# Kernel tuning notes

Measured on AMD Instinct MI355X. Metric: run time of the kernel, lower is better.

## Reference

```python
import jax, jax.numpy as jnp
import numpy as np

D_MODEL = 768
N_HEADS = 12
D_K = D_MODEL // N_HEADS

def setup_inputs() -> dict:
    key = jax.random.key(0)
    ks = jax.random.split(key, 9)
    B, S = 4, 2048
    s = 1.0 / np.sqrt(D_MODEL)
    return {
        "x": jax.random.normal(ks[0], (B, S, D_MODEL), dtype=jnp.float32),
        "Wq": jax.random.normal(ks[1], (D_MODEL, D_MODEL), dtype=jnp.float32) * s,
        "bq": jnp.zeros((D_MODEL,), dtype=jnp.float32),
        "Wk": jax.random.normal(ks[2], (D_MODEL, D_MODEL), dtype=jnp.float32) * s,
        "bk": jnp.zeros((D_MODEL,), dtype=jnp.float32),
        "Wv": jax.random.normal(ks[3], (D_MODEL, D_MODEL), dtype=jnp.float32) * s,
        "bv": jnp.zeros((D_MODEL,), dtype=jnp.float32),
        "Wo": jax.random.normal(ks[4], (D_MODEL, D_MODEL), dtype=jnp.float32) * s,
        "bo": jnp.zeros((D_MODEL,), dtype=jnp.float32),
    }

def reference(x, Wq, bq, Wk, bk, Wv, bv, Wo, bo):
    B, S, _ = x.shape
    # projections (nn.Linear: x @ W^T + b; here weights stored as (in, out) so x @ W + b)
    q = x @ Wq + bq
    k = x @ Wk + bk
    v = x @ Wv + bv
    # split heads -> (B, H, S, d_k)
    q = q.reshape(B, S, N_HEADS, D_K).transpose(0, 2, 1, 3)
    k = k.reshape(B, S, N_HEADS, D_K).transpose(0, 2, 1, 3)
    v = v.reshape(B, S, N_HEADS, D_K).transpose(0, 2, 1, 3)
    scores = jnp.einsum('bhqd,bhkd->bhqk', q, k) / jnp.sqrt(jnp.float32(D_K))
    causal = jnp.tril(jnp.ones((S, S), dtype=bool))  # True = keep
    scores = jnp.where(causal, scores, jnp.finfo(scores.dtype).min)
    weights = jax.nn.softmax(scores, axis=-1)  # dropout is identity in eval
    out = jnp.einsum('bhqk,bhkd->bhqd', weights, v)
    out = out.transpose(0, 2, 1, 3).reshape(B, S, D_MODEL)
    return out @ Wo + bo
```

## Files before the change

### kernel.cpp

```cpp
#include <hip/hip_runtime.h>
#include <hip/hip_bf16.h>

#define DM    768
#define HEADS 12
#define DK    64
#define SEQ   2048
#define BATCH 4
#define NE    ((size_t)BATCH * SEQ * DM)
#define KT    12
#define BRICK 8192

typedef short v8s __attribute__((ext_vector_type(8)));
typedef float v4f __attribute__((ext_vector_type(4)));

#define LDS_PTR(p) ((__attribute__((address_space(3))) unsigned int*)(p))
#define GLB_PTR(p) ((const __attribute__((address_space(1))) unsigned int*)(p))

__device__ __forceinline__ unsigned short f2bf(float f) {
    union { float f; unsigned u; } v; v.f = f;
    unsigned r = (v.u + 0x7FFFu + ((v.u >> 16) & 1u)) >> 16;
    return (unsigned short)r;
}
__device__ __forceinline__ unsigned pk2(float a, float b) {
    union { float f; unsigned u; } x, y; x.f = a; y.f = b;
    return (x.u >> 16) | (y.u & 0xFFFF0000u);
}
__device__ __forceinline__ unsigned pk2r(float a, float b) {
    return (unsigned)f2bf(a) | ((unsigned)f2bf(b) << 16);
}
__device__ __forceinline__ float fexp2(float x) {
#if __has_builtin(__builtin_amdgcn_exp2f)
    return __builtin_amdgcn_exp2f(x);
#else
    return __expf(x * 0.69314718056f);
#endif
}

#define QSCALE 0.18033688011112042f

__global__ __launch_bounds__(256)
void cvt_x_kernel(const float* __restrict__ x, unsigned short* __restrict__ xb) {
    const size_t p = ((size_t)blockIdx.x * 256 + threadIdx.x) * 8;
    const int m = (int)(p / DM);
    const int k = (int)(p % DM);
    const float4 a = *(const float4*)(x + p);
    const float4 b = *(const float4*)(x + p + 4);
    v8s o;
    o[0] = (short)f2bf(a.x); o[1] = (short)f2bf(a.y);
    o[2] = (short)f2bf(a.z); o[3] = (short)f2bf(a.w);
    o[4] = (short)f2bf(b.x); o[5] = (short)f2bf(b.y);
    o[6] = (short)f2bf(b.z); o[7] = (short)f2bf(b.w);
    const size_t dst = ((size_t)(m >> 7) * KT + (k >> 6)) * BRICK + (size_t)(m & 127) * 64 + (k & 63);
    *(v8s*)(xb + dst) = o;
}

__global__ __launch_bounds__(256)
void cvt_w_kernel(const float* __restrict__ W0, const float* __restrict__ W1,
                  const float* __restrict__ W2, const float* __restrict__ W3,
                  unsigned short* __restrict__ wt) {
    __shared__ unsigned short T[64][72];
    const int z = blockIdx.z;
    const float* W = (z == 0) ? W0 : (z == 1) ? W1 : (z == 2) ? W2 : W3;
    const float scale = (z == 0) ? QSCALE : 1.0f;
    const int k0 = blockIdx.x * 64, n0 = blockIdx.y * 64;
    const int t = threadIdx.x;
    {
        const int kr = t >> 2;
        const int ns = (t & 3) * 16;
        #pragma unroll
        for (int j = 0; j < 4; ++j) {
            const float4 v = *(const float4*)(W + (size_t)(k0 + kr) * DM + n0 + ns + j * 4);
            T[ns + j * 4 + 0][kr] = f2bf(v.x * scale);
            T[ns + j * 4 + 1][kr] = f2bf(v.y * scale);
            T[ns + j * 4 + 2][kr] = f2bf(v.z * scale);
            T[ns + j * 4 + 3][kr] = f2bf(v.w * scale);
        }
    }
    __syncthreads();
    {
        unsigned short* dst = wt + (size_t)z * DM * DM +
            ((size_t)(n0 >> 7) * KT + (k0 >> 6)) * BRICK + (size_t)(n0 & 64) * 64;
        const int n = t >> 2;
        const int ks = (t & 3) * 16;
        #pragma unroll
        for (int j = 0; j < 2; ++j)
            *(v8s*)(dst + (size_t)n * 64 + ks + j * 8) = *(const v8s*)&T[n][ks + j * 8];
    }
}

__global__ __launch_bounds__(256)
void gemm_qkv_kernel(const unsigned short* __restrict__ xb, const unsigned short* __restrict__ wtbuf,
                     const float* __restrict__ bq, const float* __restrict__ bk,
                     const float* __restrict__ bv,
                     unsigned short* __restrict__ qb, unsigned short* __restrict__ kb,
                     unsigned short* __restrict__ vtb) {
    __shared__ unsigned short smem[32768];
    const int idx = blockIdx.x;
    const int xcd = idx & 7, g = idx >> 3;
    const int mb = xcd + 8 * (g & 7);
    const int yb = g >> 3;
    const int z = yb / 6;
    const int N0 = (yb % 6) * 128;
    const float* bias = (z == 0) ? bq : (z == 1) ? bk : bv;
    const float bscale = (z == 0) ? QSCALE : 1.0f;

    const int t = threadIdx.x;
    const int w = t >> 6, lane = t & 63, quad = lane >> 4, l15 = lane & 15;
    const int wm = w >> 1, wn = w & 1;
    const int M0 = mb * 128;

    const unsigned short* gA = xb + (size_t)mb * (KT * BRICK);
    const unsigned short* gB = wtbuf + (size_t)yb * (KT * BRICK);

    const int r8 = lane >> 3;
    const int c8 = (lane & 7) ^ r8;
    const int goff = r8 * 64 + c8 * 8;
    const int rl = l15 & 7, rh = l15 >> 3;

    v4f acc[4][4];
    #pragma unroll
    for (int i = 0; i < 4; ++i)
        #pragma unroll
        for (int j = 0; j < 4; ++j) acc[i][j] = (v4f){0, 0, 0, 0};

    #pragma unroll
    for (int u = 0; u < 4; ++u) {
        const int win = w * 4 + u;
        __builtin_amdgcn_global_load_lds(GLB_PTR(gA + win * 512 + goff), LDS_PTR(smem + win * 512), 16, 0, 0);
        __builtin_amdgcn_global_load_lds(GLB_PTR(gB + win * 512 + goff), LDS_PTR(smem + 16384 + win * 512), 16, 0, 0);
    }
    __syncthreads();

    for (int kt = 0; kt < KT; ++kt) {
        const int cur = kt & 1;
        if (kt + 1 < KT) {
            const unsigned short* ta = gA + (kt + 1) * BRICK;
            const unsigned short* tb = gB + (kt + 1) * BRICK;
            const int nb = (1 - cur) * 8192;
            #pragma unroll
            for (int u = 0; u < 4; ++u) {
                const int win = w * 4 + u;
                __builtin_amdgcn_global_load_lds(GLB_PTR(ta + win * 512 + goff), LDS_PTR(smem + nb + win * 512), 16, 0, 0);
                __builtin_amdgcn_global_load_lds(GLB_PTR(tb + win * 512 + goff), LDS_PTR(smem + 16384 + nb + win * 512), 16, 0, 0);
            }
        }
        const unsigned short* As = smem + cur * 8192;
        const unsigned short* Bs = smem + 16384 + cur * 8192;
        #pragma unroll
        for (int kc = 0; kc < 2; ++kc) {
            const int cs = ((kc << 2) | quad) ^ rl;
            v8s a[4], b[4];
            #pragma unroll
            for (int i = 0; i < 4; ++i)
                a[i] = *(const v8s*)&As[(wm * 8 + i * 2 + rh) * 512 + rl * 64 + cs * 8];
            #pragma unroll
            for (int j = 0; j < 4; ++j)
                b[j] = *(const v8s*)&Bs[(wn * 8 + j * 2 + rh) * 512 + rl * 64 + cs * 8];
            #pragma unroll
            for (int i = 0; i < 4; ++i)
                #pragma unroll
                for (int j = 0; j < 4; ++j)
                    acc[i][j] = __builtin_amdgcn_mfma_f32_16x16x32_bf16(a[i], b[j], acc[i][j], 0, 0, 0);
        }
        __syncthreads();
    }

    const int b_ = M0 >> 11;
    const int sidx0 = M0 & 2047;
    const int h0 = N0 >> 6;

    if (z < 2) {
        unsigned short* outp = (z == 0) ? qb : kb;
        #pragma unroll
        for (int j = 0; j < 4; ++j) {
            const int n = N0 + wn * 64 + j * 16 + l15;
            const int h = n >> 6, d = n & 63;
            const float bv_ = bias[n] * bscale;
            #pragma unroll
            for (int i = 0; i < 4; ++i)
                #pragma unroll
                for (int r = 0; r < 4; ++r) {
                    const int sidx = sidx0 + wm * 64 + i * 16 + quad * 4 + r;
                    outp[(((size_t)(b_ * HEADS + h) * SEQ + sidx) << 6) + d] = f2bf(acc[i][j][r] + bv_);
                }
        }
    } else {
        unsigned short* Ts = smem;
        #pragma unroll
        for (int p = 0; p < 2; ++p) {
            __syncthreads();
            if (wm == p) {
                #pragma unroll
                for (int j = 0; j < 4; ++j) {
                    const int dloc = wn * 64 + j * 16 + l15;
                    const float bv_ = bias[N0 + dloc];
                    #pragma unroll
                    for (int i = 0; i < 4; ++i)
                        #pragma unroll
                        for (int r = 0; r < 4; ++r)
                            Ts[dloc * 72 + i * 16 + quad * 4 + r] = f2bf(acc[i][j][r] + bv_);
                }
            }
            __syncthreads();
            const int dloc = t >> 1, ms = (t & 1) * 32;
            const int h = h0 + (dloc >> 6), d = dloc & 63;
            unsigned short* dst = vtb + (((size_t)(b_ * HEADS + h) * DK + d) << 11) + sidx0 + p * 64 + ms;
            #pragma unroll
            for (int jj = 0; jj < 4; ++jj)
                *(v8s*)(dst + jj * 8) = *(const v8s*)&Ts[dloc * 72 + ms + jj * 8];
        }
    }
}

__global__ __launch_bounds__(256)
void gemm_out_kernel(const unsigned short* __restrict__ ob, const unsigned short* __restrict__ wto,
                     const float* __restrict__ bias, float* __restrict__ out) {
    __shared__ unsigned short smem[32768];
    const int idx = blockIdx.x;
    const int xcd = idx & 7, g = idx >> 3;
    const int mb = xcd + 8 * (g & 7);
    const int nb = g >> 3;
    const int t = threadIdx.x;
    const int w = t >> 6, lane = t & 63, quad = lane >> 4, l15 = lane & 15;
    const int wm = w >> 1, wn = w & 1;
    const int M0 = mb * 128;
    const int N0 = nb * 128;

    const unsigned short* gA = ob + (size_t)mb * (KT * BRICK);
    const unsigned short* gB = wto + (size_t)nb * (KT * BRICK);

    const int r8 = lane >> 3;
    const int c8 = (lane & 7) ^ r8;
    const int goff = r8 * 64 + c8 * 8;
    const int rl = l15 & 7, rh = l15 >> 3;

    v4f acc[4][4];
    #pragma unroll
    for (int i = 0; i < 4; ++i)
        #pragma unroll
        for (int j = 0; j < 4; ++j) acc[i][j] = (v4f){0, 0, 0, 0};

    #pragma unroll
    for (int u = 0; u < 4; ++u) {
        const int win = w * 4 + u;
        __builtin_amdgcn_global_load_lds(GLB_PTR(gA + win * 512 + goff), LDS_PTR(smem + win * 512), 16, 0, 0);
        __builtin_amdgcn_global_load_lds(GLB_PTR(gB + win * 512 + goff), LDS_PTR(smem + 16384 + win * 512), 16, 0, 0);
    }
    __syncthreads();

    for (int kt = 0; kt < KT; ++kt) {
        const int cur = kt & 1;
        if (kt + 1 < KT) {
            const unsigned short* ta = gA + (kt + 1) * BRICK;
            const unsigned short* tb = gB + (kt + 1) * BRICK;
            const int nxt = (1 - cur) * 8192;
            #pragma unroll
            for (int u = 0; u < 4; ++u) {
                const int win = w * 4 + u;
                __builtin_amdgcn_global_load_lds(GLB_PTR(ta + win * 512 + goff), LDS_PTR(smem + nxt + win * 512), 16, 0, 0);
                __builtin_amdgcn_global_load_lds(GLB_PTR(tb + win * 512 + goff), LDS_PTR(smem + 16384 + nxt + win * 512), 16, 0, 0);
            }
        }
        const unsigned short* As = smem + cur * 8192;
        const unsigned short* Bs = smem + 16384 + cur * 8192;
        #pragma unroll
        for (int kc = 0; kc < 2; ++kc) {
            const int cs = ((kc << 2) | quad) ^ rl;
            v8s a[4], b[4];
            #pragma unroll
            for (int i = 0; i < 4; ++i)
                a[i] = *(const v8s*)&As[(wm * 8 + i * 2 + rh) * 512 + rl * 64 + cs * 8];
            #pragma unroll
            for (int j = 0; j < 4; ++j)
                b[j] = *(const v8s*)&Bs[(wn * 8 + j * 2 + rh) * 512 + rl * 64 + cs * 8];
            #pragma unroll
            for (int i = 0; i < 4; ++i)
                #pragma unroll
                for (int j = 0; j < 4; ++j)
                    acc[i][j] = __builtin_amdgcn_mfma_f32_16x16x32_bf16(a[i], b[j], acc[i][j], 0, 0, 0);
        }
        __syncthreads();
    }

    #pragma unroll
    for (int j = 0; j < 4; ++j) {
        const int n = N0 + wn * 64 + j * 16 + l15;
        const float bv_ = bias[n];
        #pragma unroll
        for (int i = 0; i < 4; ++i)
            #pragma unroll
            for (int r = 0; r < 4; ++r) {
                const int m = M0 + wm * 64 + i * 16 + quad * 4 + r;
                out[(size_t)m * DM + n] = acc[i][j][r] + bv_;
            }
    }
}

__global__ __launch_bounds__(256, 3)
void attn_kernel(const unsigned short* __restrict__ Q, const unsigned short* __restrict__ K,
                 const unsigned short* __restrict__ VT, unsigned short* __restrict__ O) {
    __shared__ unsigned short Kb[2][64][72];
    __shared__ unsigned short Vb[2][64][72];
    __shared__ unsigned short Ps[4][16][72];
    const int t = threadIdx.x;
    const int w = t >> 6, lane = t & 63, quad = lane >> 4, l15 = lane & 15;

    const int idx = blockIdx.x;
    const int xcd = idx & 7;
    const int j   = idx >> 3;
    const int bh  = xcd + 8 * (j >> 4);
    const int s   = j & 15;
    const int sA  = s, sB = 31 - s;
    const int q0A = sA * 64, q0B = sB * 64;
    const int nkt = sB + 1;
    const size_t kvbase = (size_t)bh * SEQ * DK;

    v8s qfA[2], qfB[2];
    #pragma unroll
    for (int c = 0; c < 2; ++c) {
        qfA[c] = *(const v8s*)(Q + kvbase + (size_t)(q0A + w * 16 + l15) * DK + c * 32 + quad * 8);
        qfB[c] = *(const v8s*)(Q + kvbase + (size_t)(q0B + w * 16 + l15) * DK + c * 32 + quad * 8);
    }

    v4f oA[4], oB[4];
    #pragma unroll
    for (int nf = 0; nf < 4; ++nf) { oA[nf] = (v4f){0,0,0,0}; oB[nf] = (v4f){0,0,0,0}; }
    float lsA = 0.f, lsB = 0.f;

    const int srow = t >> 3;
    const int scol = (t & 7) * 8;

    v8s kr0 = *(const v8s*)(K  + kvbase + (size_t)srow * DK + scol);
    v8s kr1 = *(const v8s*)(K  + kvbase + (size_t)(srow + 32) * DK + scol);
    v8s vr0 = *(const v8s*)(VT + kvbase + ((size_t)srow << 11) + scol);
    v8s vr1 = *(const v8s*)(VT + kvbase + ((size_t)(srow + 32) << 11) + scol);
    *(v8s*)&Kb[0][srow][scol]      = kr0;
    *(v8s*)&Kb[0][srow + 32][scol] = kr1;
    *(v8s*)&Vb[0][srow][scol]      = vr0;
    *(v8s*)&Vb[0][srow + 32][scol] = vr1;
    __syncthreads();

    const int qA = q0A + w * 16 + l15;
    const int qB = q0B + w * 16 + l15;

    for (int kt = 0; kt < nkt; ++kt) {
        const int k0 = kt * 64;
        const int cur = kt & 1;
        if (kt + 1 < nkt) {
            const int kn = k0 + 64;
            kr0 = *(const v8s*)(K  + kvbase + (size_t)(kn + srow) * DK + scol);
            kr1 = *(const v8s*)(K  + kvbase + (size_t)(kn + srow + 32) * DK + scol);
            vr0 = *(const v8s*)(VT + kvbase + ((size_t)srow << 11) + kn + scol);
            vr1 = *(const v8s*)(VT + kvbase + ((size_t)(srow + 32) << 11) + kn + scol);
        }

        const bool actA = (kt <= sA);

        v4f scB[4], scA[4];
        #pragma unroll
        for (int s4 = 0; s4 < 4; ++s4) { scB[s4] = (v4f){0,0,0,0}; scA[s4] = (v4f){0,0,0,0}; }
        #pragma unroll
        for (int c = 0; c < 2; ++c)
            #pragma unroll
            for (int s4 = 0; s4 < 4; ++s4) {
                const v8s kf = *(const v8s*)&Kb[cur][s4 * 16 + l15][c * 32 + quad * 8];
                scB[s4] = __builtin_amdgcn_mfma_f32_16x16x32_bf16(kf, qfB[c], scB[s4], 0, 0, 0);
                if (actA)
                    scA[s4] = __builtin_amdgcn_mfma_f32_16x16x32_bf16(kf, qfA[c], scA[s4], 0, 0, 0);
            }

        {
            const bool msk = (kt == nkt - 1);
            #pragma unroll
            for (int s4 = 0; s4 < 4; ++s4) {
                float p[4];
                #pragma unroll
                for (int r = 0; r < 4; ++r) {
                    const int key = k0 + s4 * 16 + quad * 4 + r;
                    const float e = fexp2(scB[s4][r]);
                    p[r] = (!msk || key <= qB) ? e : 0.f;
                    lsB += p[r];
                }
                uint2 pkv; pkv.x = pk2(p[0], p[1]); pkv.y = pk2(p[2], p[3]);
                *(uint2*)&Ps[w][l15][s4 * 16 + quad * 4] = pkv;
            }
            #pragma unroll
            for (int kc = 0; kc < 2; ++kc) {
                const v8s pf = *(const v8s*)&Ps[w][l15][kc * 32 + quad * 8];
                #pragma unroll
                for (int nf = 0; nf < 4; ++nf) {
                    const v8s vf = *(const v8s*)&Vb[cur][nf * 16 + l15][kc * 32 + quad * 8];
                    oB[nf] = __builtin_amdgcn_mfma_f32_16x16x32_bf16(vf, pf, oB[nf], 0, 0, 0);
                }
            }
        }

        if (actA) {
            const bool msk = (kt == sA);
            #pragma unroll
            for (int s4 = 0; s4 < 4; ++s4) {
                float p[4];
                #pragma unroll
                for (int r = 0; r < 4; ++r) {
                    const int key = k0 + s4 * 16 + quad * 4 + r;
                    const float e = fexp2(scA[s4][r]);
                    p[r] = (!msk || key <= qA) ? e : 0.f;
                    lsA += p[r];
                }
                uint2 pkv; pkv.x = pk2(p[0], p[1]); pkv.y = pk2(p[2], p[3]);
                *(uint2*)&Ps[w][l15][s4 * 16 + quad * 4] = pkv;
            }
            #pragma unroll
            for (int kc = 0; kc < 2; ++kc) {
                const v8s pf = *(const v8s*)&Ps[w][l15][kc * 32 + quad * 8];
                #pragma unroll
                for (int nf = 0; nf < 4; ++nf) {
                    const v8s vf = *(const v8s*)&Vb[cur][nf * 16 + l15][kc * 32 + quad * 8];
                    oA[nf] = __builtin_amdgcn_mfma_f32_16x16x32_bf16(vf, pf, oA[nf], 0, 0, 0);
                }
            }
        }

        if (kt + 1 < nkt) {
            const int nxt = 1 - cur;
            *(v8s*)&Kb[nxt][srow][scol]      = kr0;
            *(v8s*)&Kb[nxt][srow + 32][scol] = kr1;
            *(v8s*)&Vb[nxt][srow][scol]      = vr0;
            *(v8s*)&Vb[nxt][srow + 32][scol] = vr1;
        }
        __syncthreads();
    }

    lsA += __shfl_xor(lsA, 16); lsA += __shfl_xor(lsA, 32);
    lsB += __shfl_xor(lsB, 16); lsB += __shfl_xor(lsB, 32);
    const float invA = 1.f / lsA, invB = 1.f / lsB;

    const int b = bh / HEADS, h = bh % HEADS;
    const size_t brA = ((size_t)(b * 16 + (q0A >> 7)) * KT + h) * BRICK;
    const size_t brB = ((size_t)(b * 16 + (q0B >> 7)) * KT + h) * BRICK;
    const int rowlA = (q0A & 127) + w * 16 + l15;
    const int rowlB = (q0B & 127) + w * 16 + l15;
    #pragma unroll
    for (int nf = 0; nf < 4; ++nf) {
        uint2 a2, b2;
        a2.x = pk2r(oA[nf][0] * invA, oA[nf][1] * invA);
        a2.y = pk2r(oA[nf][2] * invA, oA[nf][3] * invA);
        b2.x = pk2r(oB[nf][0] * invB, oB[nf][1] * invB);
        b2.y = pk2r(oB[nf][2] * invB, oB[nf][3] * invB);
        *(uint2*)(O + brA + (size_t)rowlA * 64 + nf * 16 + quad * 4) = a2;
        *(uint2*)(O + brB + (size_t)rowlB * 64 + nf * 16 + quad * 4) = b2;
    }
}

extern "C" void kernel_launch(void* const* d_in, const int* in_sizes, int n_in,
                              void* d_out, int out_size, void* d_ws, size_t ws_size,
                              hipStream_t stream) {
    const float* x  = (const float*)d_in[0];
    const float* Wq = (const float*)d_in[1];
    const float* bq = (const float*)d_in[2];
    const float* Wk = (const float*)d_in[3];
    const float* bk = (const float*)d_in[4];
    const float* Wv = (const float*)d_in[5];
    const float* bv = (const float*)d_in[6];
    const float* Wo = (const float*)d_in[7];
    const float* bo = (const float*)d_in[8];
    float* out = (float*)d_out;

    unsigned short* xb  = (unsigned short*)d_ws;
    unsigned short* qb  = xb  + NE;
    unsigned short* kb  = qb  + NE;
    unsigned short* vtb = kb  + NE;
    unsigned short* wt  = vtb + NE;
    unsigned short* ob  = xb;

    cvt_x_kernel<<<dim3(NE / (8 * 256)), 256, 0, stream>>>(x, xb);
    cvt_w_kernel<<<dim3(12, 12, 4), 256, 0, stream>>>(Wq, Wk, Wv, Wo, wt);
    gemm_qkv_kernel<<<dim3(1152), 256, 0, stream>>>(xb, wt, bq, bk, bv, qb, kb, vtb);
    attn_kernel<<<dim3(768), 256, 0, stream>>>(qb, kb, vtb, ob);
    gemm_out_kernel<<<dim3(384), 256, 0, stream>>>(ob, wt + (size_t)3 * DM * DM, bo, out);
}
```

Baseline: 219.3 us.

## Compute softmax row sums via MFMA with ones vector and hoist V fragment loads

```diff
diff --git a/kernel.cpp b/kernel.cpp
--- a/kernel.cpp
+++ b/kernel.cpp
@@ -325,7 +325,10 @@
     v4f oA[4], oB[4];
     #pragma unroll
     for (int nf = 0; nf < 4; ++nf) { oA[nf] = (v4f){0,0,0,0}; oB[nf] = (v4f){0,0,0,0}; }
-    float lsA = 0.f, lsB = 0.f;
+    v4f osA = (v4f){0,0,0,0}, osB = (v4f){0,0,0,0};
+
+    const short one_bf = (short)0x3F80;
+    const v8s ones = (v8s){one_bf, one_bf, one_bf, one_bf, one_bf, one_bf, one_bf, one_bf};
 
     const int srow = t >> 3;
     const int scol = (t & 7) * 8;
@@ -369,17 +372,26 @@
                     scA[s4] = __builtin_amdgcn_mfma_f32_16x16x32_bf16(kf, qfA[c], scA[s4], 0, 0, 0);
             }
 
+        v8s vfc[2][4];
+        #pragma unroll
+        for (int kc = 0; kc < 2; ++kc)
+            #pragma unroll
+            for (int nf = 0; nf < 4; ++nf)
+                vfc[kc][nf] = *(const v8s*)&Vb[cur][nf * 16 + l15][kc * 32 + quad * 8];
+
         {
             const bool msk = (kt == nkt - 1);
             #pragma unroll
             for (int s4 = 0; s4 < 4; ++s4) {
                 float p[4];
                 #pragma unroll
-                for (int r = 0; r < 4; ++r) {
-                    const int key = k0 + s4 * 16 + quad * 4 + r;
-                    const float e = fexp2(scB[s4][r]);
-                    p[r] = (!msk || key <= qB) ? e : 0.f;
-                    lsB += p[r];
+                for (int r = 0; r < 4; ++r) p[r] = fexp2(scB[s4][r]);
+                if (msk) {
+                    #pragma unroll
+                    for (int r = 0; r < 4; ++r) {
+                        const int key = k0 + s4 * 16 + quad * 4 + r;
+                        if (key > qB) p[r] = 0.f;
+                    }
                 }
                 uint2 pkv; pkv.x = pk2(p[0], p[1]); pkv.y = pk2(p[2], p[3]);
                 *(uint2*)&Ps[w][l15][s4 * 16 + quad * 4] = pkv;
@@ -387,11 +399,10 @@
             #pragma unroll
             for (int kc = 0; kc < 2; ++kc) {
                 const v8s pf = *(const v8s*)&Ps[w][l15][kc * 32 + quad * 8];
-                #pragma unroll
-                for (int nf = 0; nf < 4; ++nf) {
-                    const v8s vf = *(const v8s*)&Vb[cur][nf * 16 + l15][kc * 32 + quad * 8];
-                    oB[nf] = __builtin_amdgcn_mfma_f32_16x16x32_bf16(vf, pf, oB[nf], 0, 0, 0);
-                }
+                osB = __builtin_amdgcn_mfma_f32_16x16x32_bf16(ones, pf, osB, 0, 0, 0);
+                #pragma unroll
+                for (int nf = 0; nf < 4; ++nf)
+                    oB[nf] = __builtin_amdgcn_mfma_f32_16x16x32_bf16(vfc[kc][nf], pf, oB[nf], 0, 0, 0);
             }
         }
 
@@ -401,11 +412,13 @@
             for (int s4 = 0; s4 < 4; ++s4) {
                 float p[4];
                 #pragma unroll
-                for (int r = 0; r < 4; ++r) {
-                    const int key = k0 + s4 * 16 + quad * 4 + r;
-                    const float e = fexp2(scA[s4][r]);
-                    p[r] = (!msk || key <= qA) ? e : 0.f;
-                    lsA += p[r];
+                for (int r = 0; r < 4; ++r) p[r] = fexp2(scA[s4][r]);
+                if (msk) {
+                    #pragma unroll
+                    for (int r = 0; r < 4; ++r) {
+                        const int key = k0 + s4 * 16 + quad * 4 + r;
+                        if (key > qA) p[r] = 0.f;
+                    }
                 }
                 uint2 pkv; pkv.x = pk2(p[0], p[1]); pkv.y = pk2(p[2], p[3]);
                 *(uint2*)&Ps[w][l15][s4 * 16 + quad * 4] = pkv;
@@ -413,11 +426,10 @@
             #pragma unroll
             for (int kc = 0; kc < 2; ++kc) {
                 const v8s pf = *(const v8s*)&Ps[w][l15][kc * 32 + quad * 8];
-                #pragma unroll
-                for (int nf = 0; nf < 4; ++nf) {
-                    const v8s vf = *(const v8s*)&Vb[cur][nf * 16 + l15][kc * 32 + quad * 8];
-                    oA[nf] = __builtin_amdgcn_mfma_f32_16x16x32_bf16(vf, pf, oA[nf], 0, 0, 0);
-                }
+                osA = __builtin_amdgcn_mfma_f32_16x16x32_bf16(ones, pf, osA, 0, 0, 0);
+                #pragma unroll
+                for (int nf = 0; nf < 4; ++nf)
+                    oA[nf] = __builtin_amdgcn_mfma_f32_16x16x32_bf16(vfc[kc][nf], pf, oA[nf], 0, 0, 0);
             }
         }
 
@@ -431,9 +443,7 @@
         __syncthreads();
     }
 
-    lsA += __shfl_xor(lsA, 16); lsA += __shfl_xor(lsA, 32);
-    lsB += __shfl_xor(lsB, 16); lsB += __shfl_xor(lsB, 32);
-    const float invA = 1.f / lsA, invB = 1.f / lsB;
+    const float invA = 1.f / osA[0], invB = 1.f / osB[0];
 
     const int b = bh / HEADS, h = bh % HEADS;
     const size_t brA = ((size_t)(b * 16 + (q0A >> 7)) * KT + h) * BRICK;
```

Result: faster. 206.5 us (-5.8%).

## Split attention into one query tile per block with swizzled LDS and MFMA row sums

Applied to the files above, without the earlier changes.

```diff
diff --git a/kernel.cpp b/kernel.cpp
--- a/kernel.cpp
+++ b/kernel.cpp
@@ -296,159 +296,132 @@
     }
 }
 
-__global__ __launch_bounds__(256, 3)
+__global__ __launch_bounds__(256, 4)
 void attn_kernel(const unsigned short* __restrict__ Q, const unsigned short* __restrict__ K,
                  const unsigned short* __restrict__ VT, unsigned short* __restrict__ O) {
-    __shared__ unsigned short Kb[2][64][72];
-    __shared__ unsigned short Vb[2][64][72];
-    __shared__ unsigned short Ps[4][16][72];
+    __shared__ unsigned short Kb[2][64][64];
+    __shared__ unsigned short Vb[2][64][64];
+    __shared__ unsigned short Ps[4][16][64];
     const int t = threadIdx.x;
     const int w = t >> 6, lane = t & 63, quad = lane >> 4, l15 = lane & 15;
+    const int e7 = l15 & 7;
 
     const int idx = blockIdx.x;
     const int xcd = idx & 7;
-    const int j   = idx >> 3;
-    const int bh  = xcd + 8 * (j >> 4);
-    const int s   = j & 15;
-    const int sA  = s, sB = 31 - s;
-    const int q0A = sA * 64, q0B = sB * 64;
-    const int nkt = sB + 1;
+    const int g   = idx >> 3;
+    const int bh  = xcd + 8 * (g % 6);
+    const int s   = 31 - g / 6;
+    const int q0  = s * 64;
+    const int nkt = s + 1;
     const size_t kvbase = (size_t)bh * SEQ * DK;
 
-    v8s qfA[2], qfB[2];
-    #pragma unroll
-    for (int c = 0; c < 2; ++c) {
-        qfA[c] = *(const v8s*)(Q + kvbase + (size_t)(q0A + w * 16 + l15) * DK + c * 32 + quad * 8);
-        qfB[c] = *(const v8s*)(Q + kvbase + (size_t)(q0B + w * 16 + l15) * DK + c * 32 + quad * 8);
-    }
-
-    v4f oA[4], oB[4];
-    #pragma unroll
-    for (int nf = 0; nf < 4; ++nf) { oA[nf] = (v4f){0,0,0,0}; oB[nf] = (v4f){0,0,0,0}; }
-    float lsA = 0.f, lsB = 0.f;
+    v8s qf[2];
+    #pragma unroll
+    for (int c = 0; c < 2; ++c)
+        qf[c] = *(const v8s*)(Q + kvbase + (size_t)(q0 + w * 16 + l15) * DK + c * 32 + quad * 8);
+
+    v4f o[4];
+    #pragma unroll
+    for (int nf = 0; nf < 4; ++nf) o[nf] = (v4f){0, 0, 0, 0};
+    v4f os = (v4f){0, 0, 0, 0};
+    const v4f zero4 = (v4f){0, 0, 0, 0};
+
+    const short one_bf = (short)0x3F80;
+    const v8s ones = (v8s){one_bf, one_bf, one_bf, one_bf, one_bf, one_bf, one_bf, one_bf};
 
     const int srow = t >> 3;
-    const int scol = (t & 7) * 8;
-
-    v8s kr0 = *(const v8s*)(K  + kvbase + (size_t)srow * DK + scol);
-    v8s kr1 = *(const v8s*)(K  + kvbase + (size_t)(srow + 32) * DK + scol);
-    v8s vr0 = *(const v8s*)(VT + kvbase + ((size_t)srow << 11) + scol);
-    v8s vr1 = *(const v8s*)(VT + kvbase + ((size_t)(srow + 32) << 11) + scol);
-    *(v8s*)&Kb[0][srow][scol]      = kr0;
-    *(v8s*)&Kb[0][srow + 32][scol] = kr1;
-    *(v8s*)&Vb[0][srow][scol]      = vr0;
-    *(v8s*)&Vb[0][srow + 32][scol] = vr1;
+    const int sc16 = t & 7;
+    const int scolsw = (sc16 ^ (srow & 7)) * 8;
+    const int gcol = sc16 * 8;
+
+    v8s kr0 = *(const v8s*)(K  + kvbase + (size_t)srow * DK + gcol);
+    v8s kr1 = *(const v8s*)(K  + kvbase + (size_t)(srow + 32) * DK + gcol);
+    v8s vr0 = *(const v8s*)(VT + kvbase + ((size_t)srow << 11) + gcol);
+    v8s vr1 = *(const v8s*)(VT + kvbase + ((size_t)(srow + 32) << 11) + gcol);
+    *(v8s*)&Kb[0][srow][scolsw]      = kr0;
+    *(v8s*)&Kb[0][srow + 32][scolsw] = kr1;
+    *(v8s*)&Vb[0][srow][scolsw]      = vr0;
+    *(v8s*)&Vb[0][srow + 32][scolsw] = vr1;
     __syncthreads();
 
-    const int qA = q0A + w * 16 + l15;
-    const int qB = q0B + w * 16 + l15;
+    const int q_ = q0 + w * 16 + l15;
 
     for (int kt = 0; kt < nkt; ++kt) {
         const int k0 = kt * 64;
         const int cur = kt & 1;
         if (kt + 1 < nkt) {
             const int kn = k0 + 64;
-            kr0 = *(const v8s*)(K  + kvbase + (size_t)(kn + srow) * DK + scol);
-            kr1 = *(const v8s*)(K  + kvbase + (size_t)(kn + srow + 32) * DK + scol);
-            vr0 = *(const v8s*)(VT + kvbase + ((size_t)srow << 11) + kn + scol);
-            vr1 = *(const v8s*)(VT + kvbase + ((size_t)(srow + 32) << 11) + kn + scol);
-        }
-
-        const bool actA = (kt <= sA);
-
-        v4f scB[4], scA[4];
-        #pragma unroll
-        for (int s4 = 0; s4 < 4; ++s4) { scB[s4] = (v4f){0,0,0,0}; scA[s4] = (v4f){0,0,0,0}; }
-        #pragma unroll
-        for (int c = 0; c < 2; ++c)
-            #pragma unroll
-            for (int s4 = 0; s4 < 4; ++s4) {
-                const v8s kf = *(const v8s*)&Kb[cur][s4 * 16 + l15][c * 32 + quad * 8];
-                scB[s4] = __builtin_amdgcn_mfma_f32_16x16x32_bf16(kf, qfB[c], scB[s4], 0, 0, 0);
-                if (actA)
-                    scA[s4] = __builtin_amdgcn_mfma_f32_16x16x32_bf16(kf, qfA[c], scA[s4], 0, 0, 0);
-            }
+            kr0 = *(const v8s*)(K  + kvbase + (size_t)(kn + srow) * DK + gcol);
+            kr1 = *(const v8s*)(K  + kvbase + (size_t)(kn + srow + 32) * DK + gcol);
+            vr0 = *(const v8s*)(VT + kvbase + ((size_t)srow << 11) + kn + gcol);
+            vr1 = *(const v8s*)(VT + kvbase + ((size_t)(srow + 32) << 11) + kn + gcol);
+        }
+
+        v4f sc[4];
+        #pragma unroll
+        for (int s4 = 0; s4 < 4; ++s4) {
+            const v8s kf = *(const v8s*)&Kb[cur][s4 * 16 + l15][(quad ^ e7) * 8];
+            sc[s4] = __builtin_amdgcn_mfma_f32_16x16x32_bf16(kf, qf[0], zero4, 0, 0, 0);
+        }
+        #pragma unroll
+        for (int s4 = 0; s4 < 4; ++s4) {
+            const v8s kf = *(const v8s*)&Kb[cur][s4 * 16 + l15][((4 | quad) ^ e7) * 8];
+            sc[s4] = __builtin_amdgcn_mfma_f32_16x16x32_bf16(kf, qf[1], sc[s4], 0, 0, 0);
+        }
 
         {
-            const bool msk = (kt == nkt - 1);
+            const bool msk = (kt == s);
             #pragma unroll
             for (int s4 = 0; s4 < 4; ++s4) {
                 float p[4];
                 #pragma unroll
-                for (int r = 0; r < 4; ++r) {
-                    const int key = k0 + s4 * 16 + quad * 4 + r;
-                    const float e = fexp2(scB[s4][r]);
-                    p[r] = (!msk || key <= qB) ? e : 0.f;
-                    lsB += p[r];
+                for (int r = 0; r < 4; ++r) p[r] = fexp2(sc[s4][r]);
+                if (msk) {
+                    #pragma unroll
+                    for (int r = 0; r < 4; ++r) {
+                        const int key = k0 + s4 * 16 + quad * 4 + r;
+                        if (key > q_) p[r] = 0.f;
+                    }
                 }
                 uint2 pkv; pkv.x = pk2(p[0], p[1]); pkv.y = pk2(p[2], p[3]);
-                *(uint2*)&Ps[w][l15][s4 * 16 + quad * 4] = pkv;
-            }
-            #pragma unroll
-            for (int kc = 0; kc < 2; ++kc) {
-                const v8s pf = *(const v8s*)&Ps[w][l15][kc * 32 + quad * 8];
-                #pragma unroll
-                for (int nf = 0; nf < 4; ++nf) {
-                    const v8s vf = *(const v8s*)&Vb[cur][nf * 16 + l15][kc * 32 + quad * 8];
-                    oB[nf] = __builtin_amdgcn_mfma_f32_16x16x32_bf16(vf, pf, oB[nf], 0, 0, 0);
-                }
-            }
-        }
-
-        if (actA) {
-            const bool msk = (kt == sA);
-            #pragma unroll
-            for (int s4 = 0; s4 < 4; ++s4) {
-                float p[4];
-                #pragma unroll
-                for (int r = 0; r < 4; ++r) {
-                    const int key = k0 + s4 * 16 + quad * 4 + r;
-                    const float e = fexp2(scA[s4][r]);
-                    p[r] = (!msk || key <= qA) ? e : 0.f;
-                    lsA += p[r];
-                }
-                uint2 pkv; pkv.x = pk2(p[0], p[1]); pkv.y = pk2(p[2], p[3]);
-                *(uint2*)&Ps[w][l15][s4 * 16 + quad * 4] = pkv;
-            }
-            #pragma unroll
-            for (int kc = 0; kc < 2; ++kc) {
-                const v8s pf = *(const v8s*)&Ps[w][l15][kc * 32 + quad * 8];
-                #pragma unroll
-                for (int nf = 0; nf < 4; ++nf) {
-                    const v8s vf = *(const v8s*)&Vb[cur][nf * 16 + l15][kc * 32 + quad * 8];
-                    oA[nf] = __builtin_amdgcn_mfma_f32_16x16x32_bf16(vf, pf, oA[nf], 0, 0, 0);
-                }
+                const int col8 = (s4 * 4 + quad) ^ (e7 << 1);
+                *(uint2*)&Ps[w][l15][col8 * 4] = pkv;
+            }
+        }
+
+        #pragma unroll
+        for (int kc = 0; kc < 2; ++kc) {
+            const int c16 = ((kc * 4 + quad) ^ e7) * 8;
+            const v8s pf = *(const v8s*)&Ps[w][l15][c16];
+            os = __builtin_amdgcn_mfma_f32_16x16x32_bf16(ones, pf, os, 0, 0, 0);
+            #pragma unroll
+            for (int nf = 0; nf < 4; ++nf) {
+                const v8s vf = *(const v8s*)&Vb[cur][nf * 16 + l15][c16];
+                o[nf] = __builtin_amdgcn_mfma_f32_16x16x32_bf16(vf, pf, o[nf], 0, 0, 0);
             }
         }
 
         if (kt + 1 < nkt) {
             const int nxt = 1 - cur;
-            *(v8s*)&Kb[nxt][srow][scol]      = kr0;
-            *(v8s*)&Kb[nxt][srow + 32][scol] = kr1;
-            *(v8s*)&Vb[nxt][srow][scol]      = vr0;
-            *(v8s*)&Vb[nxt][srow + 32][scol] = vr1;
+            *(v8s*)&Kb[nxt][srow][scolsw]      = kr0;
+            *(v8s*)&Kb[nxt][srow + 32][scolsw] = kr1;
+            *(v8s*)&Vb[nxt][srow][scolsw]      = vr0;
+            *(v8s*)&Vb[nxt][srow + 32][scolsw] = vr1;
         }
         __syncthreads();
     }
 
-    lsA += __shfl_xor(lsA, 16); lsA += __shfl_xor(lsA, 32);
-    lsB += __shfl_xor(lsB, 16); lsB += __shfl_xor(lsB, 32);
-    const float invA = 1.f / lsA, invB = 1.f / lsB;
+    const float inv = 1.f / os[0];
 
     const int b = bh / HEADS, h = bh % HEADS;
-    const size_t brA = ((size_t)(b * 16 + (q0A >> 7)) * KT + h) * BRICK;
-    const size_t brB = ((size_t)(b * 16 + (q0B >> 7)) * KT + h) * BRICK;
-    const int rowlA = (q0A & 127) + w * 16 + l15;
-    const int rowlB = (q0B & 127) + w * 16 + l15;
+    const size_t br = ((size_t)(b * 16 + (q0 >> 7)) * KT + h) * BRICK;
+    const int rowl = (q0 & 127) + w * 16 + l15;
     #pragma unroll
     for (int nf = 0; nf < 4; ++nf) {
-        uint2 a2, b2;
-        a2.x = pk2r(oA[nf][0] * invA, oA[nf][1] * invA);
-        a2.y = pk2r(oA[nf][2] * invA, oA[nf][3] * invA);
-        b2.x = pk2r(oB[nf][0] * invB, oB[nf][1] * invB);
-        b2.y = pk2r(oB[nf][2] * invB, oB[nf][3] * invB);
-        *(uint2*)(O + brA + (size_t)rowlA * 64 + nf * 16 + quad * 4) = a2;
-        *(uint2*)(O + brB + (size_t)rowlB * 64 + nf * 16 + quad * 4) = b2;
+        uint2 a2;
+        a2.x = pk2r(o[nf][0] * inv, o[nf][1] * inv);
+        a2.y = pk2r(o[nf][2] * inv, o[nf][3] * inv);
+        *(uint2*)(O + br + (size_t)rowl * 64 + nf * 16 + quad * 4) = a2;
     }
 }
 
@@ -476,6 +449,6 @@
     cvt_x_kernel<<<dim3(NE / (8 * 256)), 256, 0, stream>>>(x, xb);
     cvt_w_kernel<<<dim3(12, 12, 4), 256, 0, stream>>>(Wq, Wk, Wv, Wo, wt);
     gemm_qkv_kernel<<<dim3(1152), 256, 0, stream>>>(xb, wt, bq, bk, bv, qb, kb, vtb);
-    attn_kernel<<<dim3(768), 256, 0, stream>>>(qb, kb, vtb, ob);
+    attn_kernel<<<dim3(1536), 256, 0, stream>>>(qb, kb, vtb, ob);
     gemm_out_kernel<<<dim3(384), 256, 0, stream>>>(ob, wt + (size_t)3 * DM * DM, bo, out);
 }
```

Measured after the change: 202.4 us. 1.08x faster.
